# Performance work log

Hardware: AMD Instinct MI355X
Metric: run time of the kernel (lower is better)

## Reference

```python
import jax, jax.numpy as jnp
import numpy as np

B, CH, CW, H, FH, FW = 32, 16, 16, 8, 4, 4
NQ = 64
NK = CH * FH * CW * FW  # 4096
D_IN, D_V, D_MODEL = 512, 64, 512


def setup_inputs() -> dict:
    key = jax.random.key(0)
    k1, k2, k3, k4, k5 = jax.random.split(key, 5)
    att12 = jax.random.uniform(k1, (B, CH, CW, H, FH, FW), dtype=jnp.float32)
    att3 = jax.random.uniform(k2, (B, H, NQ, CH * CW), dtype=jnp.float32)
    values = jax.random.normal(k3, (B, NK, D_IN), dtype=jnp.float32)
    # Learned params (xavier-ish scale)
    W_v = jax.random.normal(k4, (H * D_V, D_IN), dtype=jnp.float32) * (1.0 / np.sqrt(D_IN))
    b_v = jnp.zeros((H * D_V,), dtype=jnp.float32)
    W_o = jax.random.normal(k5, (D_MODEL, H * D_V), dtype=jnp.float32) * (1.0 / np.sqrt(H * D_V))
    b_o = jnp.zeros((D_MODEL,), dtype=jnp.float32)
    return {"att12": att12, "att3": att3, "values": values,
            "W_v": W_v, "b_v": b_v, "W_o": W_o, "b_o": b_o}


def reference(att12, att3, values, W_v, b_v, W_o, b_o):
    b_s, h, nq, _ = att3.shape
    ch = cw = CH
    fh, fw = att12.shape[-2:]
    nk = values.shape[1]
    d_v = W_v.shape[0] // h
    # v: [b, h, nk, d_v]
    v = (values @ W_v.T + b_v).reshape(b_s, nk, h, d_v).transpose(0, 2, 1, 3)
    # att12 -> [b, h, 1, ch, cw, fh, fw]
    a12 = jnp.transpose(att12, (0, 3, 1, 2, 4, 5))[:, :, None]
    # att3 -> [b, h, nq, ch, cw, 1, 1]
    a3 = att3.reshape(b_s, h, nq, ch, cw, 1, 1)
    # broadcast multiply, then interleave to key order (ch, fh, cw, fw)
    att = (a12 * a3).transpose(0, 1, 2, 3, 5, 4, 6).reshape(b_s, h, nq, nk)
    att = jax.nn.softmax(att, axis=-1)
    out = jnp.einsum('bhqk,bhkd->bhqd', att, v)
    out = out.transpose(0, 2, 1, 3).reshape(b_s, nq, h * d_v)
    return out @ W_o.T + b_o
```

## Files before the change

### kernel.cpp

```cpp
#include <hip/hip_runtime.h>

typedef short bf16x8 __attribute__((ext_vector_type(8)));
typedef short bf16x4 __attribute__((ext_vector_type(4)));
typedef float f32x4 __attribute__((ext_vector_type(4)));

__device__ __forceinline__ unsigned short f2bf(float f) {
  union { float f; unsigned u; } v; v.f = f;
  unsigned r = v.u + 0x7fffu + ((v.u >> 16) & 1u);
  return (unsigned short)(r >> 16);
}

__device__ __forceinline__ void gld_lds16(const void* g, void* l) {
  __builtin_amdgcn_global_load_lds(
      (const __attribute__((address_space(1))) void*)g,
      (__attribute__((address_space(3))) void*)l, 16, 0, 0);
}

__global__ __launch_bounds__(256) void convWv(const float* __restrict__ in,
                                              unsigned short* __restrict__ out) {
  long i = (long)(blockIdx.x * 256 + threadIdx.x) * 4;
  f32x4 d = *(const f32x4*)(in + i);
  bf16x4 o;
  o[0] = (short)f2bf(d[0]); o[1] = (short)f2bf(d[1]);
  o[2] = (short)f2bf(d[2]); o[3] = (short)f2bf(d[3]);
  *(bf16x4*)(out + i) = o;
}

__global__ __launch_bounds__(256) void convWo2(const float* __restrict__ in,
                                               unsigned short* __restrict__ out) {
  long i4 = (long)(blockIdx.x * 256 + threadIdx.x) * 4;
  int e = (int)(i4 >> 9), c = (int)(i4 & 511);
  f32x4 d = *(const f32x4*)(in + i4);
  bf16x4 o;
  o[0] = (short)f2bf(d[0]); o[1] = (short)f2bf(d[1]);
  o[2] = (short)f2bf(d[2]); o[3] = (short)f2bf(d[3]);
  *(bf16x4*)(out + (long)e * 1024 + c) = o;
  *(bf16x4*)(out + (long)e * 1024 + 512 + c) = o;
}

__global__ __launch_bounds__(256, 2) void vt_gemm(
    const unsigned short* __restrict__ Wvb, const float* __restrict__ V,
    unsigned short* __restrict__ vT) {
  const int t = threadIdx.x, lane = t & 63, wave = t >> 6;
  const int n0 = blockIdx.x * 128;
  const int m0 = blockIdx.y * 128;
  const int b = blockIdx.z;
  const float* Vb = V + (long)b * (4096L * 512) + (long)n0 * 512;

  __shared__ __align__(16) unsigned short As[128 * 64];
  __shared__ __align__(16) unsigned short Bs[128 * 64];

  const int wm = (wave >> 1) * 64, wn = (wave & 1) * 64;
  const int l16 = lane & 15, quad = lane >> 4;
  const int bchunk = (t & 15) * 4, brow0 = t >> 4;

  f32x4 acc[4][4];
#pragma unroll
  for (int i = 0; i < 4; ++i)
#pragma unroll
    for (int j = 0; j < 4; ++j) acc[i][j] = (f32x4){0.f, 0.f, 0.f, 0.f};

  for (int k0 = 0; k0 < 512; k0 += 64) {
#pragma unroll
    for (int s = 0; s < 4; ++s) {
      int li = s * 256 + t;
      int row = li >> 3, kq = (li & 7) * 8;
      gld_lds16(Wvb + (long)(m0 + row) * 512 + k0 + kq, (char*)As + (s * 256 + wave * 64) * 16);
    }
#pragma unroll
    for (int j = 0; j < 8; ++j) {
      int row = brow0 + 16 * j;
      f32x4 d = *(const f32x4*)(Vb + (long)row * 512 + k0 + bchunk);
      bf16x4 p;
      p[0] = (short)f2bf(d[0]); p[1] = (short)f2bf(d[1]);
      p[2] = (short)f2bf(d[2]); p[3] = (short)f2bf(d[3]);
      *(bf16x4*)(Bs + row * 64 + bchunk) = p;
    }
    __syncthreads();
#pragma unroll
    for (int ks = 0; ks < 2; ++ks) {
      bf16x8 af[4], bfv[4];
#pragma unroll
      for (int i = 0; i < 4; ++i)
        af[i] = *(const bf16x8*)(As + (wm + i * 16 + l16) * 64 + ks * 32 + quad * 8);
#pragma unroll
      for (int j = 0; j < 4; ++j)
        bfv[j] = *(const bf16x8*)(Bs + (wn + j * 16 + l16) * 64 + ks * 32 + quad * 8);
#pragma unroll
      for (int i = 0; i < 4; ++i)
#pragma unroll
        for (int j = 0; j < 4; ++j)
          acc[i][j] = __builtin_amdgcn_mfma_f32_16x16x32_bf16(af[i], bfv[j], acc[i][j], 0, 0, 0);
    }
    __syncthreads();
  }
  unsigned short* o = vT + (long)b * 2097152;
#pragma unroll
  for (int i = 0; i < 4; ++i)
#pragma unroll
    for (int j = 0; j < 4; ++j) {
      int col = n0 + wn + j * 16 + l16;
#pragma unroll
      for (int r = 0; r < 4; ++r) {
        int row = m0 + wm + i * 16 + quad * 4 + r;
        o[(long)row * 4096 + col] = f2bf(acc[i][j][r]);
      }
    }
}

__global__ __launch_bounds__(256, 2) void o_gemm(
    const float* __restrict__ att12, const float* __restrict__ att3,
    const unsigned short* __restrict__ vT, float* __restrict__ O32,
    float* __restrict__ Zp) {
  const int bh = blockIdx.x, part = blockIdx.y;
  const int b = bh >> 3, h = bh & 7;
  const int t = threadIdx.x, lane = t & 63, wave = t >> 6;

  __shared__ __align__(16) unsigned short As[4 * 64 * 32];
  __shared__ __align__(16) unsigned short Bs[4 * 64 * 32];
  __shared__ float Ored[64 * 64];
  __shared__ float Zl[4][64];

  const unsigned short* vTb = vT + (long)b * 2097152 + (long)h * 64 * 4096;
  const int gq = t & 63, gw = t >> 6;
  const float* a3row = att3 + ((long)bh * 64 + gq) * 256;
  const float* a12b = att12 + (long)b * 32768 + h * 16;
  const int l16 = lane & 15, quad = lane >> 4;
  const int kw0 = part * 2048 + gw * 512;

  f32x4 acc[4][4];
#pragma unroll
  for (int i = 0; i < 4; ++i)
#pragma unroll
    for (int j = 0; j < 4; ++j) acc[i][j] = (f32x4){0.f, 0.f, 0.f, 0.f};
  float zacc = 0.f;

  for (int it = 0; it < 16; ++it) {
#pragma unroll
    for (int s = 0; s < 4; ++s) {
      int row = t >> 2, kq = (t & 3) * 8;
      int kk = part * 2048 + s * 512 + it * 32 + kq;
      gld_lds16(vTb + (long)row * 4096 + kk, (char*)Bs + s * 4096 + wave * 1024);
    }
    {
      int kbase = kw0 + it * 32;
      int ch = kbase >> 8, fh = (kbase >> 6) & 3, cw0 = (kbase >> 2) & 15;
      f32x4 y0 = *(const f32x4*)(a3row + ch * 16 + cw0);
      f32x4 y1 = *(const f32x4*)(a3row + ch * 16 + cw0 + 4);
      const float* ap = a12b + ch * 2048 + cw0 * 128 + fh * 4;
      bf16x8 p[4];
#pragma unroll
      for (int cw = 0; cw < 8; ++cw) {
        float y = (cw < 4) ? y0[cw] : y1[cw - 4];
        f32x4 x = *(const f32x4*)(ap + cw * 128);
#pragma unroll
        for (int fw = 0; fw < 4; ++fw) {
          float e = __expf(x[fw] * y);
          zacc += e;
          p[cw >> 1][(cw & 1) * 4 + fw] = (short)f2bf(e);
        }
      }
#pragma unroll
      for (int g = 0; g < 4; ++g)
        *(bf16x8*)(As + gw * 2048 + gq * 32 + g * 8) = p[g];
    }
    __syncthreads();
    bf16x8 af[4], bfv[4];
#pragma unroll
    for (int i = 0; i < 4; ++i)
      af[i] = *(const bf16x8*)(As + wave * 2048 + (i * 16 + l16) * 32 + quad * 8);
#pragma unroll
    for (int j = 0; j < 4; ++j)
      bfv[j] = *(const bf16x8*)(Bs + wave * 2048 + (j * 16 + l16) * 32 + quad * 8);
#pragma unroll
    for (int i = 0; i < 4; ++i)
#pragma unroll
      for (int j = 0; j < 4; ++j)
        acc[i][j] = __builtin_amdgcn_mfma_f32_16x16x32_bf16(af[i], bfv[j], acc[i][j], 0, 0, 0);
    __syncthreads();
  }

  Zl[gw][gq] = zacc;
#pragma unroll
  for (int w = 0; w < 4; ++w) {
    if (wave == w) {
#pragma unroll
      for (int i = 0; i < 4; ++i)
#pragma unroll
        for (int j = 0; j < 4; ++j) {
          int col = j * 16 + l16;
#pragma unroll
          for (int r = 0; r < 4; ++r) {
            int row = i * 16 + quad * 4 + r;
            if (w == 0) Ored[row * 64 + col] = acc[i][j][r];
            else Ored[row * 64 + col] += acc[i][j][r];
          }
        }
    }
    __syncthreads();
  }
  if (t < 64) {
    float z = Zl[0][t] + Zl[1][t] + Zl[2][t] + Zl[3][t];
    Zp[(long)part * 16384 + (long)bh * 64 + t] = z;
  }
  {
    int q = t >> 2, c0 = (t & 3) * 16;
    float* op = O32 + (long)part * 1048576 + ((long)(b * 64 + q)) * 512 + h * 64 + c0;
#pragma unroll
    for (int j = 0; j < 4; ++j)
      *(f32x4*)(op + j * 4) = *(const f32x4*)(Ored + q * 64 + c0 + j * 4);
  }
}

__global__ __launch_bounds__(256) void rzcomb(const float* __restrict__ Zp,
                                              float* __restrict__ rZ) {
  int i = blockIdx.x * 256 + threadIdx.x;
  rZ[i] = 1.0f / (Zp[i] + Zp[16384 + i]);
}

__global__ __launch_bounds__(256, 2) void wo_gemm(
    const float* __restrict__ O32, const float* __restrict__ rZ,
    const float* __restrict__ b_v, const unsigned short* __restrict__ Wo2,
    const float* __restrict__ b_o, float* __restrict__ out) {
  const int t = threadIdx.x, lane = t & 63, wave = t >> 6;
  const int n0 = blockIdx.x * 128;
  const int m0 = blockIdx.y * 64;

  __shared__ __align__(16) unsigned short As[64 * 32];
  __shared__ __align__(16) unsigned short Bs[128 * 32];

  const int wm = (wave >> 1) * 32, wn = (wave & 1) * 64;
  const int l16 = lane & 15, quad = lane >> 4;
  const int arow = t >> 2, akq = (t & 3) * 8;
  const int m = m0 + arow, ab = m >> 6, aq = m & 63;

  f32x4 acc[2][4];
#pragma unroll
  for (int i = 0; i < 2; ++i)
#pragma unroll
    for (int j = 0; j < 4; ++j) acc[i][j] = (f32x4){0.f, 0.f, 0.f, 0.f};

  for (int k0 = 0; k0 < 1024; k0 += 32) {
    int part = k0 >> 9, rem = k0 & 511;
    int hh = (rem + akq) >> 6;
    const float* src = O32 + (long)part * 1048576 + (long)m * 512 + rem + akq;
    f32x4 x0 = *(const f32x4*)(src);
    f32x4 x1 = *(const f32x4*)(src + 4);
    float rz = rZ[ab * 512 + hh * 64 + aq];
    f32x4 bv0 = (f32x4){0.f, 0.f, 0.f, 0.f}, bv1 = bv0;
    if (part == 0) {
      bv0 = *(const f32x4*)(b_v + rem + akq);
      bv1 = *(const f32x4*)(b_v + rem + akq + 4);
    }
    bf16x8 pa;
#pragma unroll
    for (int j = 0; j < 4; ++j) pa[j] = (short)f2bf(x0[j] * rz + bv0[j]);
#pragma unroll
    for (int j = 0; j < 4; ++j) pa[4 + j] = (short)f2bf(x1[j] * rz + bv1[j]);
    *(bf16x8*)(As + arow * 32 + akq) = pa;
#pragma unroll
    for (int s = 0; s < 2; ++s) {
      int li = s * 256 + t;
      int row = li >> 2, kq = (li & 3) * 8;
      gld_lds16(Wo2 + (long)(n0 + row) * 1024 + k0 + kq, (char*)Bs + (s * 256 + wave * 64) * 16);
    }
    __syncthreads();
    bf16x8 af[2], bfv[4];
#pragma unroll
    for (int i = 0; i < 2; ++i)
      af[i] = *(const bf16x8*)(As + (wm + i * 16 + l16) * 32 + quad * 8);
#pragma unroll
    for (int j = 0; j < 4; ++j)
      bfv[j] = *(const bf16x8*)(Bs + (wn + j * 16 + l16) * 32 + quad * 8);
#pragma unroll
    for (int i = 0; i < 2; ++i)
#pragma unroll
      for (int j = 0; j < 4; ++j)
        acc[i][j] = __builtin_amdgcn_mfma_f32_16x16x32_bf16(af[i], bfv[j], acc[i][j], 0, 0, 0);
    __syncthreads();
  }
#pragma unroll
  for (int i = 0; i < 2; ++i)
#pragma unroll
    for (int j = 0; j < 4; ++j) {
      int col = n0 + wn + j * 16 + l16;
#pragma unroll
      for (int r = 0; r < 4; ++r) {
        int row = wm + i * 16 + quad * 4 + r;
        out[(long)(m0 + row) * 512 + col] = acc[i][j][r] + b_o[col];
      }
    }
}

extern "C" void kernel_launch(void* const* d_in, const int* in_sizes, int n_in,
                              void* d_out, int out_size, void* d_ws, size_t ws_size,
                              hipStream_t stream) {
  const float* att12 = (const float*)d_in[0];
  const float* att3  = (const float*)d_in[1];
  const float* values = (const float*)d_in[2];
  const float* W_v = (const float*)d_in[3];
  const float* b_v = (const float*)d_in[4];
  const float* W_o = (const float*)d_in[5];
  const float* b_o = (const float*)d_in[6];
  float* out = (float*)d_out;

  char* ws = (char*)d_ws;
  unsigned short* vT  = (unsigned short*)(ws);
  float*          O32 = (float*)(ws + 134217728L);
  float*          Zp  = (float*)(ws + 142606336L);
  float*          rZ  = (float*)(ws + 142737408L);
  unsigned short* Wvb = (unsigned short*)(ws + 142802944L);
  unsigned short* Wo2 = (unsigned short*)(ws + 143327232L);

  convWv<<<dim3(256), dim3(256), 0, stream>>>(W_v, Wvb);
  convWo2<<<dim3(256), dim3(256), 0, stream>>>(W_o, Wo2);

  vt_gemm<<<dim3(32, 4, 32), dim3(256), 0, stream>>>(Wvb, values, vT);

  o_gemm<<<dim3(256, 2), dim3(256), 0, stream>>>(att12, att3, vT, O32, Zp);

  rzcomb<<<dim3(64), dim3(256), 0, stream>>>(Zp, rZ);

  wo_gemm<<<dim3(4, 32), dim3(256), 0, stream>>>(O32, rZ, b_v, Wo2, b_o, out);

  (void)in_sizes; (void)n_in; (void)out_size; (void)ws_size;
}
```

Measured before the change: 635.6 us.

## Drop K-split in o_gemm, normalize in-kernel to bf16, fold bias into output GEMM

o_gemm no longer splits the key dimension across two blocks. Each block now covers all 4096 keys, sums the softmax denominators itself and writes the normalized output as bf16. This removes the rzcomb kernel, the fp32 partial outputs and the K=1024 duplicated W_o GEMM. The b_v bias is folded into a precomputed bias2 = W_o·b_v + b_o, and a generic templated bf16 GEMM with 64x64 tiles (K=512) replaces wo_gemm. vt_gemm's K tile shrinks from 64 to 32, which halves LDS per block. The cost is half as many o_gemm blocks (256), which means lower parallelism for the dominant attention kernel.

```diff
diff --git a/kernel.cpp b/kernel.cpp
--- a/kernel.cpp
+++ b/kernel.cpp
@@ -16,8 +16,8 @@
       (__attribute__((address_space(3))) void*)l, 16, 0, 0);
 }
 
-__global__ __launch_bounds__(256) void convWv(const float* __restrict__ in,
-                                              unsigned short* __restrict__ out) {
+__global__ __launch_bounds__(256) void convW(const float* __restrict__ in,
+                                             unsigned short* __restrict__ out) {
   long i = (long)(blockIdx.x * 256 + threadIdx.x) * 4;
   f32x4 d = *(const f32x4*)(in + i);
   bf16x4 o;
@@ -26,16 +26,20 @@
   *(bf16x4*)(out + i) = o;
 }
 
-__global__ __launch_bounds__(256) void convWo2(const float* __restrict__ in,
-                                               unsigned short* __restrict__ out) {
-  long i4 = (long)(blockIdx.x * 256 + threadIdx.x) * 4;
-  int e = (int)(i4 >> 9), c = (int)(i4 & 511);
-  f32x4 d = *(const f32x4*)(in + i4);
-  bf16x4 o;
-  o[0] = (short)f2bf(d[0]); o[1] = (short)f2bf(d[1]);
-  o[2] = (short)f2bf(d[2]); o[3] = (short)f2bf(d[3]);
-  *(bf16x4*)(out + (long)e * 1024 + c) = o;
-  *(bf16x4*)(out + (long)e * 1024 + 512 + c) = o;
+__global__ __launch_bounds__(256) void bias2_kernel(const float* __restrict__ Wo,
+                                                    const float* __restrict__ b_v,
+                                                    const float* __restrict__ b_o,
+                                                    float* __restrict__ bias2) {
+  int e = blockIdx.x * 256 + threadIdx.x;
+  const float* wrow = Wo + (long)e * 512;
+  float s = 0.f;
+#pragma unroll 4
+  for (int d = 0; d < 512; d += 4) {
+    f32x4 w = *(const f32x4*)(wrow + d);
+    f32x4 bv = *(const f32x4*)(b_v + d);
+    s += w[0] * bv[0] + w[1] * bv[1] + w[2] * bv[2] + w[3] * bv[3];
+  }
+  bias2[e] = s + b_o[e];
 }
 
 __global__ __launch_bounds__(256, 2) void vt_gemm(
@@ -47,12 +51,12 @@
   const int b = blockIdx.z;
   const float* Vb = V + (long)b * (4096L * 512) + (long)n0 * 512;
 
-  __shared__ __align__(16) unsigned short As[128 * 64];
-  __shared__ __align__(16) unsigned short Bs[128 * 64];
+  __shared__ __align__(16) unsigned short As[128 * 32];
+  __shared__ __align__(16) unsigned short Bs[128 * 32];
 
   const int wm = (wave >> 1) * 64, wn = (wave & 1) * 64;
   const int l16 = lane & 15, quad = lane >> 4;
-  const int bchunk = (t & 15) * 4, brow0 = t >> 4;
+  const int brow0 = t >> 3, bc4 = (t & 7) * 4;
 
   f32x4 acc[4][4];
 #pragma unroll
@@ -60,38 +64,35 @@
 #pragma unroll
     for (int j = 0; j < 4; ++j) acc[i][j] = (f32x4){0.f, 0.f, 0.f, 0.f};
 
-  for (int k0 = 0; k0 < 512; k0 += 64) {
-#pragma unroll
-    for (int s = 0; s < 4; ++s) {
+  for (int k0 = 0; k0 < 512; k0 += 32) {
+#pragma unroll
+    for (int s = 0; s < 2; ++s) {
       int li = s * 256 + t;
-      int row = li >> 3, kq = (li & 7) * 8;
+      int row = li >> 2, kq = (li & 3) * 8;
       gld_lds16(Wvb + (long)(m0 + row) * 512 + k0 + kq, (char*)As + (s * 256 + wave * 64) * 16);
     }
 #pragma unroll
-    for (int j = 0; j < 8; ++j) {
-      int row = brow0 + 16 * j;
-      f32x4 d = *(const f32x4*)(Vb + (long)row * 512 + k0 + bchunk);
+    for (int j = 0; j < 4; ++j) {
+      int row = brow0 + 32 * j;
+      f32x4 d = *(const f32x4*)(Vb + (long)row * 512 + k0 + bc4);
       bf16x4 p;
       p[0] = (short)f2bf(d[0]); p[1] = (short)f2bf(d[1]);
       p[2] = (short)f2bf(d[2]); p[3] = (short)f2bf(d[3]);
-      *(bf16x4*)(Bs + row * 64 + bchunk) = p;
-    }
-    __syncthreads();
-#pragma unroll
-    for (int ks = 0; ks < 2; ++ks) {
-      bf16x8 af[4], bfv[4];
-#pragma unroll
-      for (int i = 0; i < 4; ++i)
-        af[i] = *(const bf16x8*)(As + (wm + i * 16 + l16) * 64 + ks * 32 + quad * 8);
+      *(bf16x4*)(Bs + row * 32 + bc4) = p;
+    }
+    __syncthreads();
+    bf16x8 af[4], bfv[4];
+#pragma unroll
+    for (int i = 0; i < 4; ++i)
+      af[i] = *(const bf16x8*)(As + (wm + i * 16 + l16) * 32 + quad * 8);
+#pragma unroll
+    for (int j = 0; j < 4; ++j)
+      bfv[j] = *(const bf16x8*)(Bs + (wn + j * 16 + l16) * 32 + quad * 8);
+#pragma unroll
+    for (int i = 0; i < 4; ++i)
 #pragma unroll
       for (int j = 0; j < 4; ++j)
-        bfv[j] = *(const bf16x8*)(Bs + (wn + j * 16 + l16) * 64 + ks * 32 + quad * 8);
-#pragma unroll
-      for (int i = 0; i < 4; ++i)
-#pragma unroll
-        for (int j = 0; j < 4; ++j)
-          acc[i][j] = __builtin_amdgcn_mfma_f32_16x16x32_bf16(af[i], bfv[j], acc[i][j], 0, 0, 0);
-    }
+        acc[i][j] = __builtin_amdgcn_mfma_f32_16x16x32_bf16(af[i], bfv[j], acc[i][j], 0, 0, 0);
     __syncthreads();
   }
   unsigned short* o = vT + (long)b * 2097152;
@@ -110,23 +111,22 @@
 
 __global__ __launch_bounds__(256, 2) void o_gemm(
     const float* __restrict__ att12, const float* __restrict__ att3,
-    const unsigned short* __restrict__ vT, float* __restrict__ O32,
-    float* __restrict__ Zp) {
-  const int bh = blockIdx.x, part = blockIdx.y;
+    const unsigned short* __restrict__ vT, unsigned short* __restrict__ U) {
+  const int bh = blockIdx.x;
   const int b = bh >> 3, h = bh & 7;
   const int t = threadIdx.x, lane = t & 63, wave = t >> 6;
 
   __shared__ __align__(16) unsigned short As[4 * 64 * 32];
   __shared__ __align__(16) unsigned short Bs[4 * 64 * 32];
-  __shared__ float Ored[64 * 64];
+  __shared__ float Ored[64 * 68];
   __shared__ float Zl[4][64];
+  __shared__ float rZa[64];
 
   const unsigned short* vTb = vT + (long)b * 2097152 + (long)h * 64 * 4096;
   const int gq = t & 63, gw = t >> 6;
   const float* a3row = att3 + ((long)bh * 64 + gq) * 256;
   const float* a12b = att12 + (long)b * 32768 + h * 16;
   const int l16 = lane & 15, quad = lane >> 4;
-  const int kw0 = part * 2048 + gw * 512;
 
   f32x4 acc[4][4];
 #pragma unroll
@@ -135,15 +135,15 @@
     for (int j = 0; j < 4; ++j) acc[i][j] = (f32x4){0.f, 0.f, 0.f, 0.f};
   float zacc = 0.f;
 
-  for (int it = 0; it < 16; ++it) {
+  for (int it = 0; it < 32; ++it) {
 #pragma unroll
     for (int s = 0; s < 4; ++s) {
       int row = t >> 2, kq = (t & 3) * 8;
-      int kk = part * 2048 + s * 512 + it * 32 + kq;
+      int kk = s * 1024 + it * 32 + kq;
       gld_lds16(vTb + (long)row * 4096 + kk, (char*)Bs + s * 4096 + wave * 1024);
     }
     {
-      int kbase = kw0 + it * 32;
+      int kbase = gw * 1024 + it * 32;
       int ch = kbase >> 8, fh = (kbase >> 6) & 3, cw0 = (kbase >> 2) & 15;
       f32x4 y0 = *(const f32x4*)(a3row + ch * 16 + cw0);
       f32x4 y1 = *(const f32x4*)(a3row + ch * 16 + cw0 + 4);
@@ -181,6 +181,8 @@
   }
 
   Zl[gw][gq] = zacc;
+  __syncthreads();
+  if (t < 64) rZa[t] = 1.0f / (Zl[0][t] + Zl[1][t] + Zl[2][t] + Zl[3][t]);
 #pragma unroll
   for (int w = 0; w < 4; ++w) {
     if (wave == w) {
@@ -192,104 +194,106 @@
 #pragma unroll
           for (int r = 0; r < 4; ++r) {
             int row = i * 16 + quad * 4 + r;
-            if (w == 0) Ored[row * 64 + col] = acc[i][j][r];
-            else Ored[row * 64 + col] += acc[i][j][r];
+            if (w == 0) Ored[row * 68 + col] = acc[i][j][r];
+            else Ored[row * 68 + col] += acc[i][j][r];
           }
         }
     }
     __syncthreads();
   }
-  if (t < 64) {
-    float z = Zl[0][t] + Zl[1][t] + Zl[2][t] + Zl[3][t];
-    Zp[(long)part * 16384 + (long)bh * 64 + t] = z;
-  }
   {
-    int q = t >> 2, c0 = (t & 3) * 16;
-    float* op = O32 + (long)part * 1048576 + ((long)(b * 64 + q)) * 512 + h * 64 + c0;
-#pragma unroll
-    for (int j = 0; j < 4; ++j)
-      *(f32x4*)(op + j * 4) = *(const f32x4*)(Ored + q * 64 + c0 + j * 4);
-  }
-}
-
-__global__ __launch_bounds__(256) void rzcomb(const float* __restrict__ Zp,
-                                              float* __restrict__ rZ) {
-  int i = blockIdx.x * 256 + threadIdx.x;
-  rZ[i] = 1.0f / (Zp[i] + Zp[16384 + i]);
-}
-
-__global__ __launch_bounds__(256, 2) void wo_gemm(
-    const float* __restrict__ O32, const float* __restrict__ rZ,
-    const float* __restrict__ b_v, const unsigned short* __restrict__ Wo2,
-    const float* __restrict__ b_o, float* __restrict__ out) {
-  const int t = threadIdx.x, lane = t & 63, wave = t >> 6;
-  const int n0 = blockIdx.x * 128;
-  const int m0 = blockIdx.y * 64;
-
-  __shared__ __align__(16) unsigned short As[64 * 32];
-  __shared__ __align__(16) unsigned short Bs[128 * 32];
-
-  const int wm = (wave >> 1) * 32, wn = (wave & 1) * 64;
-  const int l16 = lane & 15, quad = lane >> 4;
-  const int arow = t >> 2, akq = (t & 3) * 8;
-  const int m = m0 + arow, ab = m >> 6, aq = m & 63;
-
-  f32x4 acc[2][4];
-#pragma unroll
-  for (int i = 0; i < 2; ++i)
-#pragma unroll
-    for (int j = 0; j < 4; ++j) acc[i][j] = (f32x4){0.f, 0.f, 0.f, 0.f};
-
-  for (int k0 = 0; k0 < 1024; k0 += 32) {
-    int part = k0 >> 9, rem = k0 & 511;
-    int hh = (rem + akq) >> 6;
-    const float* src = O32 + (long)part * 1048576 + (long)m * 512 + rem + akq;
-    f32x4 x0 = *(const f32x4*)(src);
-    f32x4 x1 = *(const f32x4*)(src + 4);
-    float rz = rZ[ab * 512 + hh * 64 + aq];
-    f32x4 bv0 = (f32x4){0.f, 0.f, 0.f, 0.f}, bv1 = bv0;
-    if (part == 0) {
-      bv0 = *(const f32x4*)(b_v + rem + akq);
-      bv1 = *(const f32x4*)(b_v + rem + akq + 4);
-    }
-    bf16x8 pa;
-#pragma unroll
-    for (int j = 0; j < 4; ++j) pa[j] = (short)f2bf(x0[j] * rz + bv0[j]);
-#pragma unroll
-    for (int j = 0; j < 4; ++j) pa[4 + j] = (short)f2bf(x1[j] * rz + bv1[j]);
-    *(bf16x8*)(As + arow * 32 + akq) = pa;
-#pragma unroll
-    for (int s = 0; s < 2; ++s) {
+    int q = t >> 2, dv0 = (t & 3) * 16;
+    float rz = rZa[q];
+    unsigned short* up = U + ((long)(b * 64 + q)) * 512 + h * 64 + dv0;
+    bf16x8 o0, o1;
+#pragma unroll
+    for (int j = 0; j < 8; ++j) o0[j] = (short)f2bf(Ored[q * 68 + dv0 + j] * rz);
+#pragma unroll
+    for (int j = 0; j < 8; ++j) o1[j] = (short)f2bf(Ored[q * 68 + dv0 + 8 + j] * rz);
+    *(bf16x8*)(up) = o0;
+    *(bf16x8*)(up + 8) = o1;
+  }
+}
+
+template <int BM, int BN, bool OUT_BF16, bool ADD_BIAS>
+__global__ __launch_bounds__(256, 2) void gemm_bt(
+    const unsigned short* __restrict__ A, const unsigned short* __restrict__ Bt,
+    void* __restrict__ C, const float* __restrict__ bias,
+    int K, int lda, int ldb, int ldc) {
+  constexpr int BK = 32;
+  const int t = threadIdx.x;
+  const int lane = t & 63;
+  const int wave = t >> 6;
+  const int m0 = blockIdx.y * BM;
+  const int n0 = blockIdx.x * BN;
+
+  A += (long)m0 * lda;
+  Bt += (long)n0 * ldb;
+
+  __shared__ __align__(16) unsigned short As[BM * BK];
+  __shared__ __align__(16) unsigned short Bs[BN * BK];
+
+  constexpr int TM = BM / 32;
+  constexpr int TN = BN / 32;
+  const int wm = (wave >> 1) * (BM / 2);
+  const int wn = (wave & 1) * (BN / 2);
+  const int l16 = lane & 15;
+  const int quad = lane >> 4;
+
+  f32x4 acc[TM][TN];
+#pragma unroll
+  for (int i = 0; i < TM; ++i)
+#pragma unroll
+    for (int j = 0; j < TN; ++j) acc[i][j] = (f32x4){0.f, 0.f, 0.f, 0.f};
+
+  constexpr int ASHOT = (BM * 4) / 256;
+  constexpr int BSHOT = (BN * 4) / 256;
+
+  for (int k0 = 0; k0 < K; k0 += BK) {
+#pragma unroll
+    for (int s = 0; s < ASHOT; ++s) {
       int li = s * 256 + t;
       int row = li >> 2, kq = (li & 3) * 8;
-      gld_lds16(Wo2 + (long)(n0 + row) * 1024 + k0 + kq, (char*)Bs + (s * 256 + wave * 64) * 16);
-    }
-    __syncthreads();
-    bf16x8 af[2], bfv[4];
-#pragma unroll
-    for (int i = 0; i < 2; ++i)
-      af[i] = *(const bf16x8*)(As + (wm + i * 16 + l16) * 32 + quad * 8);
-#pragma unroll
-    for (int j = 0; j < 4; ++j)
-      bfv[j] = *(const bf16x8*)(Bs + (wn + j * 16 + l16) * 32 + quad * 8);
-#pragma unroll
-    for (int i = 0; i < 2; ++i)
-#pragma unroll
-      for (int j = 0; j < 4; ++j)
+      gld_lds16(A + (long)row * lda + k0 + kq, (char*)As + (s * 256 + wave * 64) * 16);
+    }
+#pragma unroll
+    for (int s = 0; s < BSHOT; ++s) {
+      int li = s * 256 + t;
+      int row = li >> 2, kq = (li & 3) * 8;
+      gld_lds16(Bt + (long)row * ldb + k0 + kq, (char*)Bs + (s * 256 + wave * 64) * 16);
+    }
+    __syncthreads();
+    bf16x8 af[TM], bfv[TN];
+#pragma unroll
+    for (int i = 0; i < TM; ++i)
+      af[i] = *(const bf16x8*)(As + (wm + i * 16 + l16) * BK + quad * 8);
+#pragma unroll
+    for (int j = 0; j < TN; ++j)
+      bfv[j] = *(const bf16x8*)(Bs + (wn + j * 16 + l16) * BK + quad * 8);
+#pragma unroll
+    for (int i = 0; i < TM; ++i)
+#pragma unroll
+      for (int j = 0; j < TN; ++j)
         acc[i][j] = __builtin_amdgcn_mfma_f32_16x16x32_bf16(af[i], bfv[j], acc[i][j], 0, 0, 0);
     __syncthreads();
   }
-#pragma unroll
-  for (int i = 0; i < 2; ++i)
-#pragma unroll
-    for (int j = 0; j < 4; ++j) {
-      int col = n0 + wn + j * 16 + l16;
+
+#pragma unroll
+  for (int i = 0; i < TM; ++i) {
+#pragma unroll
+    for (int j = 0; j < TN; ++j) {
+      int col = wn + j * 16 + l16;
 #pragma unroll
       for (int r = 0; r < 4; ++r) {
         int row = wm + i * 16 + quad * 4 + r;
-        out[(long)(m0 + row) * 512 + col] = acc[i][j][r] + b_o[col];
+        float v = acc[i][j][r];
+        if (ADD_BIAS) v += bias[n0 + col];
+        long idx = (long)(m0 + row) * ldc + (n0 + col);
+        if (OUT_BF16) ((unsigned short*)C)[idx] = f2bf(v);
+        else ((float*)C)[idx] = v;
       }
     }
+  }
 }
 
 extern "C" void kernel_launch(void* const* d_in, const int* in_sizes, int n_in,
@@ -305,23 +309,22 @@
   float* out = (float*)d_out;
 
   char* ws = (char*)d_ws;
-  unsigned short* vT  = (unsigned short*)(ws);
-  float*          O32 = (float*)(ws + 134217728L);
-  float*          Zp  = (float*)(ws + 142606336L);
-  float*          rZ  = (float*)(ws + 142737408L);
-  unsigned short* Wvb = (unsigned short*)(ws + 142802944L);
-  unsigned short* Wo2 = (unsigned short*)(ws + 143327232L);
-
-  convWv<<<dim3(256), dim3(256), 0, stream>>>(W_v, Wvb);
-  convWo2<<<dim3(256), dim3(256), 0, stream>>>(W_o, Wo2);
+  unsigned short* vT    = (unsigned short*)(ws);
+  unsigned short* U     = (unsigned short*)(ws + 134217728L);
+  unsigned short* Wvb   = (unsigned short*)(ws + 136314880L);
+  unsigned short* Wob   = (unsigned short*)(ws + 136839168L);
+  float*          bias2 = (float*)(ws + 137363456L);
+
+  convW<<<dim3(256), dim3(256), 0, stream>>>(W_v, Wvb);
+  convW<<<dim3(256), dim3(256), 0, stream>>>(W_o, Wob);
+  bias2_kernel<<<dim3(2), dim3(256), 0, stream>>>(W_o, b_v, b_o, bias2);
 
   vt_gemm<<<dim3(32, 4, 32), dim3(256), 0, stream>>>(Wvb, values, vT);
 
-  o_gemm<<<dim3(256, 2), dim3(256), 0, stream>>>(att12, att3, vT, O32, Zp);
-
-  rzcomb<<<dim3(64), dim3(256), 0, stream>>>(Zp, rZ);
-
-  wo_gemm<<<dim3(4, 32), dim3(256), 0, stream>>>(O32, rZ, b_v, Wo2, b_o, out);
+  o_gemm<<<dim3(256), dim3(256), 0, stream>>>(att12, att3, vT, U);
+
+  gemm_bt<64, 64, false, true><<<dim3(8, 32), dim3(256), 0, stream>>>(
+      U, Wob, out, bias2, 512, 512, 512, 512);
 
   (void)in_sizes; (void)n_in; (void)out_size; (void)ws_size;
 }
```

New measurement: 556.3 us. 12.5% less time.
